# Optimization experiments

Measured on AMD Instinct MI355X. Metric: run time of the kernel, lower is better.

Reference implementation:

```python
import jax, jax.numpy as jnp
import numpy as np

N_LAYERS = 4
GAMMA = 0.5
D_MODEL = 256
D_STATE = 64
D_CONV = 4
EXPAND = 2
D_INNER = EXPAND * D_MODEL            # 512 (= headdim, so nheads = 1)
NHEADS = 1
CONV_DIM = D_INNER + 2 * D_STATE      # 640
D_IN_PROJ = 2 * D_INNER + 2 * D_STATE + NHEADS  # 1153
VOCAB = 100
VOCAB_PAD = 104                        # padded to multiple of 8 by MambaConfig
BATCH = 8
SEQ = 2048


def setup_inputs() -> dict:
    key = jax.random.key(0)
    ks = jax.random.split(key, 8)
    def nrm(k, shape):
        # gamma init: std = 1 / d1**gamma, d1 = shape[0]
        return (jax.random.normal(k, shape, jnp.float32) * (1.0 / shape[0] ** GAMMA))
    inp = {}
    inp["input_ids"] = jax.random.randint(ks[0], (BATCH, SEQ), 0, VOCAB)
    inp["embed"] = nrm(ks[1], (VOCAB_PAD, D_MODEL))          # tied embedding / lm_head
    inp["in_proj_w"] = nrm(ks[2], (N_LAYERS * D_IN_PROJ, D_MODEL)).reshape(N_LAYERS, D_IN_PROJ, D_MODEL)
    inp["conv_w"] = nrm(ks[3], (N_LAYERS * CONV_DIM, D_CONV)).reshape(N_LAYERS, CONV_DIM, D_CONV)
    inp["conv_b"] = jnp.zeros((N_LAYERS, CONV_DIM), jnp.float32)
    inp["dt_bias"] = jax.random.uniform(ks[4], (N_LAYERS, NHEADS), jnp.float32, -4.0, -1.0)
    inp["A_log"] = jnp.log(jax.random.uniform(ks[5], (N_LAYERS, NHEADS), jnp.float32, 1.0, 16.0))
    inp["Dparam"] = jnp.ones((N_LAYERS, NHEADS), jnp.float32)
    inp["norm_g_w"] = jnp.ones((N_LAYERS, D_INNER), jnp.float32)
    inp["out_proj_w"] = nrm(ks[6], (N_LAYERS * D_MODEL, D_INNER)).reshape(N_LAYERS, D_MODEL, D_INNER)
    inp["block_norm_w"] = jnp.ones((N_LAYERS, D_MODEL), jnp.float32)
    inp["norm_f_w"] = jnp.ones((D_MODEL,), jnp.float32)
    return inp


def rmsnorm(x, w, eps=1e-5):
    return x * jax.lax.rsqrt(jnp.mean(x * x, axis=-1, keepdims=True) + eps) * w


def ssm_scan(x, dt, A, Bc, Cc):
    # x: (B,L,P)  dt: (B,L)  A: scalar  Bc,Cc: (B,L,N). Sequential selective scan.
    def step(h, inp):  # h: (B,P,N)
        x_t, dt_t, b_t, c_t = inp
        h = h * jnp.exp(dt_t * A)[:, None, None] + (dt_t[:, None] * x_t)[:, :, None] * b_t[:, None, :]
        y = jnp.einsum('bpn,bn->bp', h, c_t)
        return h, y
    h0 = jnp.zeros((x.shape[0], x.shape[2], Bc.shape[2]), x.dtype)
    xs = (jnp.swapaxes(x, 0, 1), jnp.swapaxes(dt, 0, 1), jnp.swapaxes(Bc, 0, 1), jnp.swapaxes(Cc, 0, 1))
    _, ys = jax.lax.scan(step, h0, xs)
    return jnp.swapaxes(ys, 0, 1)  # (B,L,P)


def mamba2_mixer(h, ipw, cw, cb, dtb, alog, dp, ngw, opw):
    zxbcdt = h @ ipw.T                                   # (B,L,1153)
    z = zxbcdt[..., :D_INNER]
    xBC = zxbcdt[..., D_INNER:D_INNER + CONV_DIM]
    dt_raw = zxbcdt[..., D_INNER + CONV_DIM:]            # (B,L,1)
    # depthwise causal conv1d (kernel D_CONV) + SiLU
    xp = jnp.pad(xBC, ((0, 0), (D_CONV - 1, 0), (0, 0)))
    L = xBC.shape[1]
    conv = sum(xp[:, k:k + L, :] * cw[:, k] for k in range(D_CONV)) + cb
    xBC = jax.nn.silu(conv)
    x = xBC[..., :D_INNER]
    Bc = xBC[..., D_INNER:D_INNER + D_STATE]
    Cc = xBC[..., D_INNER + D_STATE:]
    dt = jax.nn.softplus(dt_raw[..., 0] + dtb[0])        # (B,L), nheads=1
    A = -jnp.exp(alog[0])
    y = ssm_scan(x, dt, A, Bc, Cc) + dp[0] * x
    y = rmsnorm(y * jax.nn.silu(z), ngw)                 # RMSNormGated (norm after gate)
    return y @ opw.T


def reference(input_ids, embed, in_proj_w, conv_w, conv_b, dt_bias, A_log, Dparam,
              norm_g_w, out_proj_w, block_norm_w, norm_f_w):
    hidden = embed[input_ids]                            # (B,L,D_MODEL)
    residual = None
    for i in range(N_LAYERS):
        residual = hidden if residual is None else hidden + residual
        hidden = rmsnorm(residual, block_norm_w[i])
        hidden = mamba2_mixer(hidden, in_proj_w[i], conv_w[i], conv_b[i], dt_bias[i],
                              A_log[i], Dparam[i], norm_g_w[i], out_proj_w[i])
    residual = hidden + residual
    final = rmsnorm(residual, norm_f_w)
    logits = final @ embed.T                             # tied lm_head, (B,L,VOCAB_PAD)
    return logits[:, -1, :VOCAB]                         # last-token logits, (B,VOCAB)
```

## Files before the change

kernel.cpp:

```cpp
#include <hip/hip_runtime.h>
#include <math.h>

#define NB    8
#define LSEQ  2048
#define TKN   16384
#define DM    256
#define DI    512
#define DS    64
#define DIP   1153
#define DIPP  1160
#define CDIM  640
#define NL    4
#define NC    16
#define CL    128
#define VOC   100

typedef short bf16x8 __attribute__((ext_vector_type(8)));
typedef short bf16x4 __attribute__((ext_vector_type(4)));
typedef float f32x4  __attribute__((ext_vector_type(4)));
typedef unsigned short ushort_t;

__device__ __forceinline__ float block_reduce_sum256(float v) {
  __shared__ float sred[4];
  #pragma unroll
  for (int off = 32; off > 0; off >>= 1) v += __shfl_down(v, off, 64);
  int lane = threadIdx.x & 63, wid = threadIdx.x >> 6;
  if (lane == 0) sred[wid] = v;
  __syncthreads();
  return sred[0] + sred[1] + sred[2] + sred[3];
}

__device__ __forceinline__ unsigned short f2bf(float f) {
  unsigned int u = __float_as_uint(f);
  unsigned int r = u + 0x7FFFu + ((u >> 16) & 1u);
  return (unsigned short)(r >> 16);
}
__device__ __forceinline__ float bf2f(unsigned short u) {
  return __uint_as_float(((unsigned int)u) << 16);
}

__global__ __launch_bounds__(256) void convert_w(const float* __restrict__ ipw,
    const float* __restrict__ opw, ushort_t* __restrict__ wbi, ushort_t* __restrict__ wbo) {
  const int n1 = NL * DIP * DM;
  const int n2 = NL * DM * DI;
  int i4 = (blockIdx.x * 256 + threadIdx.x) * 4;
  if (i4 < n1) {
    float4 v = *(const float4*)(ipw + i4);
    bf16x4 o; o[0] = (short)f2bf(v.x); o[1] = (short)f2bf(v.y);
    o[2] = (short)f2bf(v.z); o[3] = (short)f2bf(v.w);
    *(bf16x4*)(wbi + i4) = o;
  } else {
    int j = i4 - n1;
    if (j < n2) {
      float4 v = *(const float4*)(opw + j);
      bf16x4 o; o[0] = (short)f2bf(v.x); o[1] = (short)f2bf(v.y);
      o[2] = (short)f2bf(v.z); o[3] = (short)f2bf(v.w);
      *(bf16x4*)(wbo + j) = o;
    }
  }
}

__global__ __launch_bounds__(256) void embed_rmsnorm(float* __restrict__ resid,
    ushort_t* __restrict__ hn, const float* __restrict__ w,
    const int* __restrict__ ids, const float* __restrict__ embed) {
  int wave = threadIdx.x >> 6, lane = threadIdx.x & 63;
  int t = blockIdx.x * 4 + wave;
  size_t o = (size_t)t * DM + lane * 4;
  int id = ids[t];
  float4 r4 = *(const float4*)&embed[(size_t)id * DM + lane * 4];
  *(float4*)&resid[o] = r4;
  float ss = r4.x * r4.x + r4.y * r4.y + r4.z * r4.z + r4.w * r4.w;
  #pragma unroll
  for (int m = 32; m >= 1; m >>= 1) ss += __shfl_xor(ss, m, 64);
  float sc = rsqrtf(ss * (1.f / DM) + 1e-5f);
  float4 w4 = *(const float4*)&w[lane * 4];
  bf16x4 o4;
  o4[0] = (short)f2bf(r4.x * sc * w4.x);
  o4[1] = (short)f2bf(r4.y * sc * w4.y);
  o4[2] = (short)f2bf(r4.z * sc * w4.z);
  o4[3] = (short)f2bf(r4.w * sc * w4.w);
  *(bf16x4*)&hn[o] = o4;
}

#define LSTR  40
#define LSTR2 72
__global__ __launch_bounds__(256) void gemm_nt_bf16(const ushort_t* __restrict__ A,
    const ushort_t* __restrict__ Bw, ushort_t* __restrict__ C, int N, int K, int ldc) {
  __shared__ short sA[128 * LSTR2];
  __shared__ short sB[128 * LSTR2];
  int tid = threadIdx.x;
  int bn = blockIdx.x * 128;
  int bm = blockIdx.y * 128;
  int wave = tid >> 6, lane = tid & 63;
  int wm = (wave >> 1) * 64, wn = (wave & 1) * 64;
  int q = lane >> 4, c = lane & 15;

  f32x4 acc[4][4];
  #pragma unroll
  for (int i = 0; i < 4; ++i)
    #pragma unroll
    for (int j = 0; j < 4; ++j) acc[i][j] = (f32x4)0.f;

  int sr = tid >> 1;
  int sc = (tid & 1) * 32;
  const ushort_t* Ag = A + (size_t)(bm + sr) * K + sc;
  const ushort_t* Bg = Bw + (size_t)(bn + sr) * K + sc;
  bool bok = (bn + sr) < N;
  short* sAp = &sA[sr * LSTR2 + sc];
  short* sBp = &sB[sr * LSTR2 + sc];

  for (int k0 = 0; k0 < K; k0 += 64) {
    bf16x8 a0 = *(const bf16x8*)(Ag + k0);
    bf16x8 a1 = *(const bf16x8*)(Ag + k0 + 8);
    bf16x8 a2 = *(const bf16x8*)(Ag + k0 + 16);
    bf16x8 a3 = *(const bf16x8*)(Ag + k0 + 24);
    bf16x8 b0 = (bf16x8)(short)0, b1 = (bf16x8)(short)0;
    bf16x8 b2 = (bf16x8)(short)0, b3 = (bf16x8)(short)0;
    if (bok) {
      b0 = *(const bf16x8*)(Bg + k0);
      b1 = *(const bf16x8*)(Bg + k0 + 8);
      b2 = *(const bf16x8*)(Bg + k0 + 16);
      b3 = *(const bf16x8*)(Bg + k0 + 24);
    }
    __syncthreads();
    *(bf16x8*)(sAp)      = a0;
    *(bf16x8*)(sAp + 8)  = a1;
    *(bf16x8*)(sAp + 16) = a2;
    *(bf16x8*)(sAp + 24) = a3;
    *(bf16x8*)(sBp)      = b0;
    *(bf16x8*)(sBp + 8)  = b1;
    *(bf16x8*)(sBp + 16) = b2;
    *(bf16x8*)(sBp + 24) = b3;
    __syncthreads();
    #pragma unroll
    for (int ks = 0; ks < 2; ++ks) {
      bf16x8 af[4], bfr[4];
      #pragma unroll
      for (int i = 0; i < 4; ++i)
        af[i] = *(const bf16x8*)&sA[(wm + i * 16 + c) * LSTR2 + ks * 32 + q * 8];
      #pragma unroll
      for (int j = 0; j < 4; ++j)
        bfr[j] = *(const bf16x8*)&sB[(wn + j * 16 + c) * LSTR2 + ks * 32 + q * 8];
      #pragma unroll
      for (int i = 0; i < 4; ++i)
        #pragma unroll
        for (int j = 0; j < 4; ++j)
          acc[i][j] = __builtin_amdgcn_mfma_f32_16x16x32_bf16(af[i], bfr[j], acc[i][j], 0, 0, 0);
    }
  }
  #pragma unroll
  for (int i = 0; i < 4; ++i) {
    int m = bm + wm + i * 16 + q * 4;
    #pragma unroll
    for (int j = 0; j < 4; ++j) {
      int n = bn + wn + j * 16 + c;
      if (n < N) {
        #pragma unroll
        for (int r = 0; r < 4; ++r)
          C[(size_t)(m + r) * ldc + n] = f2bf(acc[i][j][r]);
      }
    }
  }
}

__global__ __launch_bounds__(256) void outproj_norm(const ushort_t* __restrict__ yb,
    const ushort_t* __restrict__ zx, const ushort_t* __restrict__ Bw,
    const float* __restrict__ gw, float* __restrict__ resid,
    const float* __restrict__ wnext, ushort_t* __restrict__ hn) {
  __shared__ short sA[32 * LSTR];
  __shared__ short sB[256 * LSTR];
  __shared__ float swl[DI];
  __shared__ float swn[DM];
  __shared__ float rs[128];
  __shared__ float rs2[32 * 2];
  int tid = threadIdx.x;
  int bm = blockIdx.x * 32;
  int wave = tid >> 6, lane = tid & 63;
  int wm = (wave >> 1) * 16, wn = (wave & 1) * 128;
  int q = lane >> 4, c = lane & 15;
  swl[tid] = gw[tid];
  swl[tid + 256] = gw[tid + 256];
  swn[tid] = wnext[tid];

  f32x4 acc[8];
  #pragma unroll
  for (int j = 0; j < 8; ++j) acc[j] = (f32x4)0.f;

  int ar = tid >> 2, ak = (tid & 3) * 8;
  bool isa = tid < 128;
  const ushort_t* yrow = yb + (size_t)(bm + ar) * DI + ak;
  const ushort_t* zrow = zx + (size_t)(bm + ar) * DIPP + ak;
  const ushort_t* Bg = Bw + (size_t)tid * DI;
  float sumsq = 0.f;
  __syncthreads();

  for (int k0 = 0; k0 < DI; k0 += 32) {
    bf16x8 g8;
    if (isa) {
      bf16x8 y8 = *(const bf16x8*)(yrow + k0);
      bf16x8 z8 = *(const bf16x8*)(zrow + k0);
      #pragma unroll
      for (int e = 0; e < 8; ++e) {
        float zz = bf2f((ushort_t)z8[e]);
        float gg = bf2f((ushort_t)y8[e]) * (zz / (1.f + __expf(-zz)));
        sumsq += gg * gg;
        g8[e] = (short)f2bf(gg * swl[k0 + ak + e]);
      }
    }
    bf16x8 b0 = *(const bf16x8*)(Bg + k0);
    bf16x8 b1 = *(const bf16x8*)(Bg + k0 + 8);
    bf16x8 b2 = *(const bf16x8*)(Bg + k0 + 16);
    bf16x8 b3 = *(const bf16x8*)(Bg + k0 + 24);
    __syncthreads();
    if (isa) *(bf16x8*)&sA[ar * LSTR + ak] = g8;
    *(bf16x8*)&sB[tid * LSTR]      = b0;
    *(bf16x8*)&sB[tid * LSTR + 8]  = b1;
    *(bf16x8*)&sB[tid * LSTR + 16] = b2;
    *(bf16x8*)&sB[tid * LSTR + 24] = b3;
    __syncthreads();
    bf16x8 af = *(const bf16x8*)&sA[(wm + c) * LSTR + q * 8];
    #pragma unroll
    for (int j = 0; j < 8; ++j) {
      bf16x8 bfr = *(const bf16x8*)&sB[(wn + j * 16 + c) * LSTR + q * 8];
      acc[j] = __builtin_amdgcn_mfma_f32_16x16x32_bf16(af, bfr, acc[j], 0, 0, 0);
    }
  }
  if (isa) rs[tid] = sumsq;
  __syncthreads();

  float outv[8][4];
  float sq2[4];
  #pragma unroll
  for (int r = 0; r < 4; ++r) {
    int row = wm + q * 4 + r;
    float s1 = rsqrtf((rs[row * 4] + rs[row * 4 + 1] + rs[row * 4 + 2] + rs[row * 4 + 3])
                      * (1.f / DI) + 1e-5f);
    float sq = 0.f;
    #pragma unroll
    for (int j = 0; j < 8; ++j) {
      int col = wn + j * 16 + c;
      size_t ro = (size_t)(bm + row) * DM + col;
      float rn = resid[ro] + s1 * acc[j][r];
      resid[ro] = rn;
      outv[j][r] = rn;
      sq += rn * rn;
    }
    sq2[r] = sq;
  }
  #pragma unroll
  for (int r = 0; r < 4; ++r) {
    #pragma unroll
    for (int m = 1; m <= 8; m <<= 1) sq2[r] += __shfl_xor(sq2[r], m, 64);
  }
  if (c == 0) {
    #pragma unroll
    for (int r = 0; r < 4; ++r)
      rs2[(wm + q * 4 + r) * 2 + (wave & 1)] = sq2[r];
  }
  __syncthreads();
  #pragma unroll
  for (int r = 0; r < 4; ++r) {
    int row = wm + q * 4 + r;
    float s2 = rsqrtf((rs2[row * 2] + rs2[row * 2 + 1]) * (1.f / DM) + 1e-5f);
    #pragma unroll
    for (int j = 0; j < 8; ++j) {
      int col = wn + j * 16 + c;
      hn[(size_t)(bm + row) * DM + col] = f2bf(outv[j][r] * s2 * swn[col]);
    }
  }
}

__global__ __launch_bounds__(256) void conv_silu(const ushort_t* __restrict__ zx,
    const float* __restrict__ cw, const float* __restrict__ cb,
    const float* __restrict__ dtb, ushort_t* __restrict__ xo,
    ushort_t* __restrict__ Bo, ushort_t* __restrict__ Co, ushort_t* __restrict__ Ut) {
  __shared__ ushort_t tile[67 * 128];
  __shared__ ushort_t tt[128 * 72];
  __shared__ float sdt[64];
  int tid = threadIdx.x;
  int ct = blockIdx.x, tb_ = blockIdx.y, b = blockIdx.z;
  int c0 = ct * 128, l0 = tb_ * 64;
  size_t rowb = (size_t)b * LSEQ;
  bool isx = (ct < 4);
  for (int slot = tid; slot < 67 * 16; slot += 256) {
    int r = slot >> 4, gg = slot & 15;
    int l = l0 + r - 3;
    bf16x8 v = (bf16x8)(short)0;
    if (l >= 0) v = *(const bf16x8*)&zx[(rowb + l) * DIPP + DI + c0 + gg * 8];
    *(bf16x8*)&tile[r * 128 + gg * 8] = v;
  }
  if (isx && tid < 64) sdt[tid] = dtb[rowb + l0 + tid];
  int g = tid & 15, tq = tid >> 4;
  int cbase = c0 + g * 8;
  float w[4][8], bias[8];
  #pragma unroll
  for (int e = 0; e < 8; ++e) {
    float4 wv = *(const float4*)&cw[(cbase + e) * 4];
    w[0][e] = wv.x; w[1][e] = wv.y; w[2][e] = wv.z; w[3][e] = wv.w;
    bias[e] = cb[cbase + e];
  }
  __syncthreads();
  bf16x8 rows[7];
  #pragma unroll
  for (int r = 0; r < 7; ++r)
    rows[r] = *(const bf16x8*)&tile[(tq * 4 + r) * 128 + g * 8];
  #pragma unroll
  for (int it = 0; it < 4; ++it) {
    int t = tq * 4 + it;
    size_t tl = rowb + l0 + t;
    float dtv = isx ? sdt[t] : 0.f;
    bf16x8 o;
    #pragma unroll
    for (int e = 0; e < 8; ++e) {
      float s = bias[e]
              + w[0][e] * bf2f((ushort_t)rows[it][e])
              + w[1][e] * bf2f((ushort_t)rows[it + 1][e])
              + w[2][e] * bf2f((ushort_t)rows[it + 2][e])
              + w[3][e] * bf2f((ushort_t)rows[it + 3][e]);
      float v = s / (1.f + __expf(-s));
      o[e] = (short)f2bf(v);
      if (isx) tt[(g * 8 + e) * 72 + t] = f2bf(v * dtv);
    }
    if (isx) {
      *(bf16x8*)&xo[tl * DI + cbase] = o;
    } else if (g < 8) {
      *(bf16x8*)&Bo[tl * DS + (cbase - DI)] = o;
    } else {
      *(bf16x8*)&Co[tl * DS + (cbase - DI - DS)] = o;
    }
  }
  if (isx) {
    __syncthreads();
    #pragma unroll
    for (int pass = 0; pass < 4; ++pass) {
      int slot = pass * 256 + tid;
      int op = slot >> 3, sg = slot & 7;
      bf16x8 v = *(const bf16x8*)&tt[op * 72 + sg * 8];
      *(bf16x8*)&Ut[((size_t)b * DI + c0 + op) * LSEQ + l0 + sg * 8] = v;
    }
  }
}

__global__ __launch_bounds__(256) void csum_k(const ushort_t* __restrict__ zx,
    const float* __restrict__ dtbias, float* __restrict__ dtb, float* __restrict__ csumb) {
  int tid = threadIdx.x;
  int wave = tid >> 6, lane = tid & 63;
  int cg = blockIdx.x * 4 + wave;
  int b = cg >> 4, ch = cg & 15;
  size_t base = (size_t)b * LSEQ + ch * CL;
  float bias = dtbias[0];
  float x0 = bf2f(zx[(base + 2 * lane) * DIPP + (DIP - 1)]) + bias;
  float x1 = bf2f(zx[(base + 2 * lane + 1) * DIPP + (DIP - 1)]) + bias;
  float d0 = (x0 > 20.f) ? x0 : log1pf(__expf(x0));
  float d1 = (x1 > 20.f) ? x1 : log1pf(__expf(x1));
  dtb[base + 2 * lane] = d0;
  dtb[base + 2 * lane + 1] = d1;
  float p = d0 + d1;
  #pragma unroll
  for (int off = 1; off < 64; off <<= 1) {
    float t = __shfl_up(p, off, 64);
    if (lane >= off) p += t;
  }
  csumb[base + 2 * lane]     = p - d1;
  csumb[base + 2 * lane + 1] = p;
}

__global__ __launch_bounds__(256) void state_gemm(const ushort_t* __restrict__ Bb,
    const ushort_t* __restrict__ Ut, const float* __restrict__ csumb,
    const float* __restrict__ alog, float* __restrict__ hst) {
  __shared__ short sW[64 * 144];
  __shared__ short sX[128 * 40];
  __shared__ float scs[128];
  int tid = threadIdx.x;
  int ph = blockIdx.x, ch = blockIdx.y, b = blockIdx.z;
  int bc = b * NC + ch;
  size_t tb = (size_t)b * LSEQ + ch * CL;
  float Aval = -expf(alog[0]);
  if (tid < 128) scs[tid] = csumb[tb + tid];
  __syncthreads();
  float Stot = scs[127];
  {
    int s = tid >> 1, noff = (tid & 1) * 32;
    float scale = __expf(Aval * (Stot - scs[s]));
    #pragma unroll
    for (int blk = 0; blk < 4; ++blk) {
      bf16x8 v = *(const bf16x8*)&Bb[(tb + s) * DS + noff + blk * 8];
      #pragma unroll
      for (int e = 0; e < 8; ++e)
        sW[(noff + blk * 8 + e) * 144 + s] = (short)f2bf(bf2f((ushort_t)v[e]) * scale);
    }
  }
  int wave = tid >> 6, lane = tid & 63;
  int wn = (wave >> 1) * 32, wp = (wave & 1) * 64;
  int q = lane >> 4, c = lane & 15;
  f32x4 acc[2][4];
  #pragma unroll
  for (int i = 0; i < 2; ++i)
    #pragma unroll
    for (int j = 0; j < 4; ++j) acc[i][j] = (f32x4)0.f;

  for (int ks = 0; ks < 4; ++ks) {
    __syncthreads();
    {
      int r = tid >> 1, off = (tid & 1) * 16;
      size_t ua = ((size_t)b * DI + ph * 128 + r) * LSEQ + ch * CL + ks * 32 + off;
      bf16x8 u0 = *(const bf16x8*)&Ut[ua];
      bf16x8 u1 = *(const bf16x8*)&Ut[ua + 8];
      *(bf16x8*)&sX[r * 40 + off]     = u0;
      *(bf16x8*)&sX[r * 40 + off + 8] = u1;
    }
    __syncthreads();
    bf16x8 af[2], bfr[4];
    #pragma unroll
    for (int i = 0; i < 2; ++i)
      af[i] = *(const bf16x8*)&sW[(wn + i * 16 + c) * 144 + ks * 32 + q * 8];
    #pragma unroll
    for (int j = 0; j < 4; ++j)
      bfr[j] = *(const bf16x8*)&sX[(wp + j * 16 + c) * 40 + q * 8];
    #pragma unroll
    for (int i = 0; i < 2; ++i)
      #pragma unroll
      for (int j = 0; j < 4; ++j)
        acc[i][j] = __builtin_amdgcn_mfma_f32_16x16x32_bf16(af[i], bfr[j], acc[i][j], 0, 0, 0);
  }
  #pragma unroll
  for (int i = 0; i < 2; ++i) {
    int n = wn + i * 16 + q * 4;
    #pragma unroll
    for (int j = 0; j < 4; ++j) {
      int pg = ph * 128 + wp + j * 16 + c;
      #pragma unroll
      for (int r = 0; r < 4; ++r)
        hst[((size_t)bc * DS + n + r) * DI + pg] = acc[i][j][r];
    }
  }
}

__global__ __launch_bounds__(256) void combine2(const float* __restrict__ hst,
    const float* __restrict__ csumb, const float* __restrict__ alog,
    ushort_t* __restrict__ hin) {
  __shared__ ushort_t ts[64 * 17];
  int tid = threadIdx.x;
  int pt = blockIdx.x, nt = blockIdx.y, b = blockIdx.z;
  int p0 = pt * 64, n0 = nt * 16;
  int pl = tid & 63, ng = tid >> 6;
  float Aval = -expf(alog[0]);
  float h[4];
  #pragma unroll
  for (int i = 0; i < 4; ++i) h[i] = 0.f;
  for (int c = 0; c < NC; ++c) {
    int bc = b * NC + c;
    #pragma unroll
    for (int i = 0; i < 4; ++i)
      ts[pl * 17 + ng * 4 + i] = f2bf(h[i]);
    __syncthreads();
    {
      int on = tid & 15;
      #pragma unroll
      for (int pass = 0; pass < 4; ++pass) {
        int op = (tid >> 4) + pass * 16;
        hin[((size_t)bc * DI + p0 + op) * DS + n0 + on] = ts[op * 17 + on];
      }
    }
    __syncthreads();
    float Sc = csumb[(size_t)b * LSEQ + c * CL + CL - 1];
    float dec = __expf(Aval * Sc);
    #pragma unroll
    for (int i = 0; i < 4; ++i) {
      float loc = hst[((size_t)bc * DS + n0 + ng * 4 + i) * DI + p0 + pl];
      h[i] = h[i] * dec + loc;
    }
  }
}

__global__ __launch_bounds__(256) void y_gemm(const ushort_t* __restrict__ Bb,
    const ushort_t* __restrict__ Cb, const ushort_t* __restrict__ Ut,
    const ushort_t* __restrict__ hin, const float* __restrict__ csumb,
    const float* __restrict__ alog, const float* __restrict__ dpar,
    const ushort_t* __restrict__ xb, ushort_t* __restrict__ y) {
  __shared__ short sC[128 * 72];
  __shared__ short sM[128 * 136];
  __shared__ short sU[128 * 80];
  __shared__ float scs[128];
  int tid = threadIdx.x;
  int ph = blockIdx.x, ch = blockIdx.y, b = blockIdx.z;
  int bc = b * NC + ch;
  size_t tb = (size_t)b * LSEQ + ch * CL;
  float Aval = -expf(alog[0]);
  float dp = dpar[0];
  int wave = tid >> 6, lane = tid & 63;
  int q = lane >> 4, c = lane & 15;

  {
    int r = tid >> 1, off = (tid & 1) * 32;
    #pragma unroll
    for (int blk = 0; blk < 4; ++blk) {
      *(bf16x8*)&sC[r * 72 + off + blk * 8] = *(const bf16x8*)&Cb[(tb + r) * DS + off + blk * 8];
      *(bf16x8*)&sU[r * 80 + off + blk * 8] = *(const bf16x8*)&Bb[(tb + r) * DS + off + blk * 8];
    }
  }
  if (tid < 128) scs[tid] = csumb[tb + tid];
  __syncthreads();

  {
    int wm = (wave >> 1) * 64, wss = (wave & 1) * 64;
    if (wave == 1) {
      #pragma unroll
      for (int i = 0; i < 4; ++i) {
        #pragma unroll
        for (int r = 0; r < 4; ++r) {
          int t = i * 16 + q * 4 + r;
          #pragma unroll
          for (int j = 0; j < 4; ++j)
            sM[t * 136 + 64 + j * 16 + c] = 0;
        }
      }
    } else {
      f32x4 g[4][4];
      #pragma unroll
      for (int i = 0; i < 4; ++i)
        #pragma unroll
        for (int j = 0; j < 4; ++j) g[i][j] = (f32x4)0.f;
      #pragma unroll
      for (int k0 = 0; k0 < 64; k0 += 32) {
        bf16x8 af[4], bfr[4];
        #pragma unroll
        for (int i = 0; i < 4; ++i)
          af[i] = *(const bf16x8*)&sC[(wm + i * 16 + c) * 72 + k0 + q * 8];
        #pragma unroll
        for (int j = 0; j < 4; ++j)
          bfr[j] = *(const bf16x8*)&sU[(wss + j * 16 + c) * 80 + k0 + q * 8];
        #pragma unroll
        for (int i = 0; i < 4; ++i)
          #pragma unroll
          for (int j = 0; j < 4; ++j)
            g[i][j] = __builtin_amdgcn_mfma_f32_16x16x32_bf16(af[i], bfr[j], g[i][j], 0, 0, 0);
      }
      #pragma unroll
      for (int i = 0; i < 4; ++i) {
        #pragma unroll
        for (int r = 0; r < 4; ++r) {
          int t = wm + i * 16 + q * 4 + r;
          float ct = scs[t];
          #pragma unroll
          for (int j = 0; j < 4; ++j) {
            int s = wss + j * 16 + c;
            float v = g[i][j][r];
            float m = (s <= t) ? v * __expf(Aval * (ct - scs[s])) : 0.f;
            sM[t * 136 + s] = (short)f2bf(m);
          }
        }
      }
    }
  }

  int wm2 = (wave >> 1) * 64, wp = (wave & 1) * 64;
  f32x4 acc[4][4];
  #pragma unroll
  for (int i = 0; i < 4; ++i)
    #pragma unroll
    for (int j = 0; j < 4; ++j) acc[i][j] = (f32x4)0.f;

  for (int ks = 0; ks < 4; ++ks) {
    __syncthreads();
    {
      int r = tid >> 1, off = (tid & 1) * 16;
      size_t ua = ((size_t)b * DI + ph * 128 + r) * LSEQ + ch * CL + ks * 32 + off;
      bf16x8 u0 = *(const bf16x8*)&Ut[ua];
      bf16x8 u1 = *(const bf16x8*)&Ut[ua + 8];
      *(bf16x8*)&sU[r * 40 + off]     = u0;
      *(bf16x8*)&sU[r * 40 + off + 8] = u1;
    }
    __syncthreads();
    if (!(wm2 == 0 && ks >= 2)) {
      bf16x8 af[4], bfr[4];
      #pragma unroll
      for (int i = 0; i < 4; ++i)
        af[i] = *(const bf16x8*)&sM[(wm2 + i * 16 + c) * 136 + ks * 32 + q * 8];
      #pragma unroll
      for (int j = 0; j < 4; ++j)
        bfr[j] = *(const bf16x8*)&sU[(wp + j * 16 + c) * 40 + q * 8];
      #pragma unroll
      for (int i = 0; i < 4; ++i)
        #pragma unroll
        for (int j = 0; j < 4; ++j)
          acc[i][j] = __builtin_amdgcn_mfma_f32_16x16x32_bf16(af[i], bfr[j], acc[i][j], 0, 0, 0);
    }
  }

  __syncthreads();
  {
    int r = tid >> 1, off = (tid & 1) * 32;
    float sc_t = __expf(Aval * scs[r]);
    #pragma unroll
    for (int blk = 0; blk < 4; ++blk) {
      bf16x8 v = *(const bf16x8*)&sC[r * 72 + off + blk * 8];
      bf16x8 o;
      #pragma unroll
      for (int e = 0; e < 8; ++e)
        o[e] = (short)f2bf(bf2f((ushort_t)v[e]) * sc_t);
      *(bf16x8*)&sM[r * 80 + off + blk * 8] = o;
    }
  }
  for (int ks = 4; ks < 6; ++ks) {
    __syncthreads();
    {
      int r = tid >> 1, off = (tid & 1) * 16;
      size_t ha = ((size_t)bc * DI + ph * 128 + r) * DS + (ks - 4) * 32 + off;
      bf16x8 h0 = *(const bf16x8*)&hin[ha];
      bf16x8 h1 = *(const bf16x8*)&hin[ha + 8];
      *(bf16x8*)&sU[r * 40 + off]     = h0;
      *(bf16x8*)&sU[r * 40 + off + 8] = h1;
    }
    __syncthreads();
    bf16x8 af[4], bfr[4];
    #pragma unroll
    for (int i = 0; i < 4; ++i)
      af[i] = *(const bf16x8*)&sM[(wm2 + i * 16 + c) * 80 + (ks - 4) * 32 + q * 8];
    #pragma unroll
    for (int j = 0; j < 4; ++j)
      bfr[j] = *(const bf16x8*)&sU[(wp + j * 16 + c) * 40 + q * 8];
    #pragma unroll
    for (int i = 0; i < 4; ++i)
      #pragma unroll
      for (int j = 0; j < 4; ++j)
        acc[i][j] = __builtin_amdgcn_mfma_f32_16x16x32_bf16(af[i], bfr[j], acc[i][j], 0, 0, 0);
  }

  #pragma unroll
  for (int i = 0; i < 4; ++i) {
    #pragma unroll
    for (int r = 0; r < 4; ++r) {
      int t = wm2 + i * 16 + q * 4 + r;
      size_t row = (tb + t) * DI;
      #pragma unroll
      for (int j = 0; j < 4; ++j) {
        int pg = ph * 128 + wp + j * 16 + c;
        y[row + pg] = f2bf(acc[i][j][r] + dp * bf2f(xb[row + pg]));
      }
    }
  }
}

__global__ __launch_bounds__(256) void finalize(const ushort_t* __restrict__ hn,
    const float* __restrict__ embed, float* __restrict__ out) {
  int b = blockIdx.x, tid = threadIdx.x;
  __shared__ float fin[DM];
  size_t off = ((size_t)b * LSEQ + (LSEQ - 1)) * DM;
  fin[tid] = bf2f(hn[off + tid]);
  __syncthreads();
  if (tid < VOC) {
    float acc = 0.f;
    #pragma unroll 8
    for (int d = 0; d < DM; ++d) acc += fin[d] * embed[(size_t)tid * DM + d];
    out[b * VOC + tid] = acc;
  }
}

extern "C" void kernel_launch(void* const* d_in, const int* in_sizes, int n_in,
                              void* d_out, int out_size, void* d_ws, size_t ws_size,
                              hipStream_t stream) {
  const int*   ids   = (const int*)d_in[0];
  const float* embed = (const float*)d_in[1];
  const float* ipw   = (const float*)d_in[2];
  const float* cw    = (const float*)d_in[3];
  const float* cb    = (const float*)d_in[4];
  const float* dtbias= (const float*)d_in[5];
  const float* alog  = (const float*)d_in[6];
  const float* dpar  = (const float*)d_in[7];
  const float* ngw   = (const float*)d_in[8];
  const float* opw   = (const float*)d_in[9];
  const float* bnw   = (const float*)d_in[10];
  const float* nfw   = (const float*)d_in[11];
  float* out = (float*)d_out;

  char* p = (char*)d_ws;
  float* resid = (float*)p;            p += (size_t)TKN * DM * 4;
  ushort_t* hn = (ushort_t*)p;         p += (size_t)TKN * DM * 2;
  ushort_t* zx = (ushort_t*)p;         p += (size_t)TKN * DIPP * 2;
  float* dtb   = (float*)p;            p += (size_t)TKN * 4;
  float* csumb = (float*)p;            p += (size_t)TKN * 4;
  ushort_t* xb = (ushort_t*)p;         p += (size_t)TKN * DI * 2;
  ushort_t* yb = (ushort_t*)p;         p += (size_t)TKN * DI * 2;
  ushort_t* Bb = (ushort_t*)p;         p += (size_t)TKN * DS * 2;
  ushort_t* Cb = (ushort_t*)p;         p += (size_t)TKN * DS * 2;
  ushort_t* Ut = (ushort_t*)p;         p += (size_t)TKN * DI * 2;
  ushort_t* hin= (ushort_t*)p;         p += (size_t)NB * NC * DI * DS * 2;
  ushort_t* wbi= (ushort_t*)p;         p += (size_t)NL * DIP * DM * 2;
  ushort_t* wbo= (ushort_t*)p;         p += (size_t)NL * DM * DI * 2;
  float* hst = (float*)yb;

  convert_w<<<(NL * DIP * DM + NL * DM * DI + 1023) / 1024, 256, 0, stream>>>(
      ipw, opw, wbi, wbo);
  embed_rmsnorm<<<TKN / 4, 256, 0, stream>>>(resid, hn, bnw, ids, embed);

  for (int i = 0; i < NL; ++i) {
    gemm_nt_bf16<<<dim3((DIP + 127) / 128, TKN / 128), 256, 0, stream>>>(
        hn, wbi + (size_t)i * DIP * DM, zx, DIP, DM, DIPP);
    csum_k<<<32, 256, 0, stream>>>(zx, dtbias + i, dtb, csumb);
    conv_silu<<<dim3(CDIM / 128, LSEQ / 64, NB), 256, 0, stream>>>(
        zx, cw + (size_t)i * CDIM * 4, cb + (size_t)i * CDIM, dtb, xb, Bb, Cb, Ut);
    state_gemm<<<dim3(4, NC, NB), 256, 0, stream>>>(Bb, Ut, csumb, alog + i, hst);
    combine2<<<dim3(DI / 64, 4, NB), 256, 0, stream>>>(hst, csumb, alog + i, hin);
    y_gemm<<<dim3(4, NC, NB), 256, 0, stream>>>(Bb, Cb, Ut, hin, csumb, alog + i,
                                                dpar + i, xb, yb);
    const float* wnext = (i < NL - 1) ? (bnw + (size_t)(i + 1) * DM) : nfw;
    outproj_norm<<<TKN / 32, 256, 0, stream>>>(
        yb, zx, wbo + (size_t)i * DM * DI, ngw + (size_t)i * DI, resid, wnext, hn);
  }

  finalize<<<NB, 256, 0, stream>>>(hn, embed, out);
}
```

Baseline: 562.5 us.

## Fold dt cumsum into conv kernel and merge prologue kernels

The weight-conversion and embedding+RMSNorm kernels become one prologue launch. The separate dt softplus/cumsum kernel becomes extra blocks inside conv_silu. To remove the ordering dependency between them, the dt scaling moves out of the transposed x buffer and into state_gemm (state scale) and y_gemm (intra-chunk mask), which now read dt per position. This saves five kernel launches and their serialisation gaps, at the cost of some idle blocks in the conv grid and a slightly different bf16 rounding point for x*dt.

```diff
diff --git a/kernel.cpp b/kernel.cpp
--- a/kernel.cpp
+++ b/kernel.cpp
@@ -20,16 +20,6 @@
 typedef float f32x4  __attribute__((ext_vector_type(4)));
 typedef unsigned short ushort_t;
 
-__device__ __forceinline__ float block_reduce_sum256(float v) {
-  __shared__ float sred[4];
-  #pragma unroll
-  for (int off = 32; off > 0; off >>= 1) v += __shfl_down(v, off, 64);
-  int lane = threadIdx.x & 63, wid = threadIdx.x >> 6;
-  if (lane == 0) sred[wid] = v;
-  __syncthreads();
-  return sred[0] + sred[1] + sred[2] + sred[3];
-}
-
 __device__ __forceinline__ unsigned short f2bf(float f) {
   unsigned int u = __float_as_uint(f);
   unsigned int r = u + 0x7FFFu + ((u >> 16) & 1u);
@@ -39,47 +29,48 @@
   return __uint_as_float(((unsigned int)u) << 16);
 }
 
-__global__ __launch_bounds__(256) void convert_w(const float* __restrict__ ipw,
-    const float* __restrict__ opw, ushort_t* __restrict__ wbi, ushort_t* __restrict__ wbo) {
-  const int n1 = NL * DIP * DM;
-  const int n2 = NL * DM * DI;
-  int i4 = (blockIdx.x * 256 + threadIdx.x) * 4;
-  if (i4 < n1) {
-    float4 v = *(const float4*)(ipw + i4);
-    bf16x4 o; o[0] = (short)f2bf(v.x); o[1] = (short)f2bf(v.y);
-    o[2] = (short)f2bf(v.z); o[3] = (short)f2bf(v.w);
-    *(bf16x4*)(wbi + i4) = o;
+__global__ __launch_bounds__(256) void prologue(const float* __restrict__ ipw,
+    const float* __restrict__ opw, ushort_t* __restrict__ wbi, ushort_t* __restrict__ wbo,
+    const int* __restrict__ ids, const float* __restrict__ embed,
+    float* __restrict__ resid, ushort_t* __restrict__ hn, const float* __restrict__ w0) {
+  int blk = blockIdx.x;
+  if (blk < TKN / 4) {
+    int wave = threadIdx.x >> 6, lane = threadIdx.x & 63;
+    int t = blk * 4 + wave;
+    size_t o = (size_t)t * DM + lane * 4;
+    int id = ids[t];
+    float4 r4 = *(const float4*)&embed[(size_t)id * DM + lane * 4];
+    *(float4*)&resid[o] = r4;
+    float ss = r4.x * r4.x + r4.y * r4.y + r4.z * r4.z + r4.w * r4.w;
+    #pragma unroll
+    for (int m = 32; m >= 1; m >>= 1) ss += __shfl_xor(ss, m, 64);
+    float sc = rsqrtf(ss * (1.f / DM) + 1e-5f);
+    float4 w4 = *(const float4*)&w0[lane * 4];
+    bf16x4 o4;
+    o4[0] = (short)f2bf(r4.x * sc * w4.x);
+    o4[1] = (short)f2bf(r4.y * sc * w4.y);
+    o4[2] = (short)f2bf(r4.z * sc * w4.z);
+    o4[3] = (short)f2bf(r4.w * sc * w4.w);
+    *(bf16x4*)&hn[o] = o4;
   } else {
-    int j = i4 - n1;
-    if (j < n2) {
-      float4 v = *(const float4*)(opw + j);
+    const int n1 = NL * DIP * DM;
+    const int n2 = NL * DM * DI;
+    int i4 = ((blk - TKN / 4) * 256 + threadIdx.x) * 4;
+    if (i4 < n1) {
+      float4 v = *(const float4*)(ipw + i4);
       bf16x4 o; o[0] = (short)f2bf(v.x); o[1] = (short)f2bf(v.y);
       o[2] = (short)f2bf(v.z); o[3] = (short)f2bf(v.w);
-      *(bf16x4*)(wbo + j) = o;
-    }
-  }
-}
-
-__global__ __launch_bounds__(256) void embed_rmsnorm(float* __restrict__ resid,
-    ushort_t* __restrict__ hn, const float* __restrict__ w,
-    const int* __restrict__ ids, const float* __restrict__ embed) {
-  int wave = threadIdx.x >> 6, lane = threadIdx.x & 63;
-  int t = blockIdx.x * 4 + wave;
-  size_t o = (size_t)t * DM + lane * 4;
-  int id = ids[t];
-  float4 r4 = *(const float4*)&embed[(size_t)id * DM + lane * 4];
-  *(float4*)&resid[o] = r4;
-  float ss = r4.x * r4.x + r4.y * r4.y + r4.z * r4.z + r4.w * r4.w;
-  #pragma unroll
-  for (int m = 32; m >= 1; m >>= 1) ss += __shfl_xor(ss, m, 64);
-  float sc = rsqrtf(ss * (1.f / DM) + 1e-5f);
-  float4 w4 = *(const float4*)&w[lane * 4];
-  bf16x4 o4;
-  o4[0] = (short)f2bf(r4.x * sc * w4.x);
-  o4[1] = (short)f2bf(r4.y * sc * w4.y);
-  o4[2] = (short)f2bf(r4.z * sc * w4.z);
-  o4[3] = (short)f2bf(r4.w * sc * w4.w);
-  *(bf16x4*)&hn[o] = o4;
+      *(bf16x4*)(wbi + i4) = o;
+    } else {
+      int j = i4 - n1;
+      if (j < n2) {
+        float4 v = *(const float4*)(opw + j);
+        bf16x4 o; o[0] = (short)f2bf(v.x); o[1] = (short)f2bf(v.y);
+        o[2] = (short)f2bf(v.z); o[3] = (short)f2bf(v.w);
+        *(bf16x4*)(wbo + j) = o;
+      }
+    }
+  }
 }
 
 #define LSTR  40
@@ -272,15 +263,37 @@
 
 __global__ __launch_bounds__(256) void conv_silu(const ushort_t* __restrict__ zx,
     const float* __restrict__ cw, const float* __restrict__ cb,
-    const float* __restrict__ dtb, ushort_t* __restrict__ xo,
-    ushort_t* __restrict__ Bo, ushort_t* __restrict__ Co, ushort_t* __restrict__ Ut) {
+    const float* __restrict__ dtbias, ushort_t* __restrict__ xo,
+    ushort_t* __restrict__ Bo, ushort_t* __restrict__ Co, ushort_t* __restrict__ Ut,
+    float* __restrict__ dtb, float* __restrict__ csumb) {
   __shared__ ushort_t tile[67 * 128];
   __shared__ ushort_t tt[128 * 72];
-  __shared__ float sdt[64];
   int tid = threadIdx.x;
   int ct = blockIdx.x, tb_ = blockIdx.y, b = blockIdx.z;
+  size_t rowb = (size_t)b * LSEQ;
+  if (ct == 5) {
+    if (tb_ < 16 && tid < 64) {
+      int lane = tid;
+      size_t base = rowb + (size_t)tb_ * CL;
+      float bias = dtbias[0];
+      float x0 = bf2f(zx[(base + 2 * lane) * DIPP + (DIP - 1)]) + bias;
+      float x1 = bf2f(zx[(base + 2 * lane + 1) * DIPP + (DIP - 1)]) + bias;
+      float d0 = (x0 > 20.f) ? x0 : log1pf(__expf(x0));
+      float d1 = (x1 > 20.f) ? x1 : log1pf(__expf(x1));
+      dtb[base + 2 * lane] = d0;
+      dtb[base + 2 * lane + 1] = d1;
+      float p = d0 + d1;
+      #pragma unroll
+      for (int off = 1; off < 64; off <<= 1) {
+        float t = __shfl_up(p, off, 64);
+        if (lane >= off) p += t;
+      }
+      csumb[base + 2 * lane]     = p - d1;
+      csumb[base + 2 * lane + 1] = p;
+    }
+    return;
+  }
   int c0 = ct * 128, l0 = tb_ * 64;
-  size_t rowb = (size_t)b * LSEQ;
   bool isx = (ct < 4);
   for (int slot = tid; slot < 67 * 16; slot += 256) {
     int r = slot >> 4, gg = slot & 15;
@@ -289,7 +302,6 @@
     if (l >= 0) v = *(const bf16x8*)&zx[(rowb + l) * DIPP + DI + c0 + gg * 8];
     *(bf16x8*)&tile[r * 128 + gg * 8] = v;
   }
-  if (isx && tid < 64) sdt[tid] = dtb[rowb + l0 + tid];
   int g = tid & 15, tq = tid >> 4;
   int cbase = c0 + g * 8;
   float w[4][8], bias[8];
@@ -308,7 +320,6 @@
   for (int it = 0; it < 4; ++it) {
     int t = tq * 4 + it;
     size_t tl = rowb + l0 + t;
-    float dtv = isx ? sdt[t] : 0.f;
     bf16x8 o;
     #pragma unroll
     for (int e = 0; e < 8; ++e) {
@@ -319,7 +330,7 @@
               + w[3][e] * bf2f((ushort_t)rows[it + 3][e]);
       float v = s / (1.f + __expf(-s));
       o[e] = (short)f2bf(v);
-      if (isx) tt[(g * 8 + e) * 72 + t] = f2bf(v * dtv);
+      if (isx) tt[(g * 8 + e) * 72 + t] = (ushort_t)o[e];
     }
     if (isx) {
       *(bf16x8*)&xo[tl * DI + cbase] = o;
@@ -341,47 +352,25 @@
   }
 }
 
-__global__ __launch_bounds__(256) void csum_k(const ushort_t* __restrict__ zx,
-    const float* __restrict__ dtbias, float* __restrict__ dtb, float* __restrict__ csumb) {
-  int tid = threadIdx.x;
-  int wave = tid >> 6, lane = tid & 63;
-  int cg = blockIdx.x * 4 + wave;
-  int b = cg >> 4, ch = cg & 15;
-  size_t base = (size_t)b * LSEQ + ch * CL;
-  float bias = dtbias[0];
-  float x0 = bf2f(zx[(base + 2 * lane) * DIPP + (DIP - 1)]) + bias;
-  float x1 = bf2f(zx[(base + 2 * lane + 1) * DIPP + (DIP - 1)]) + bias;
-  float d0 = (x0 > 20.f) ? x0 : log1pf(__expf(x0));
-  float d1 = (x1 > 20.f) ? x1 : log1pf(__expf(x1));
-  dtb[base + 2 * lane] = d0;
-  dtb[base + 2 * lane + 1] = d1;
-  float p = d0 + d1;
-  #pragma unroll
-  for (int off = 1; off < 64; off <<= 1) {
-    float t = __shfl_up(p, off, 64);
-    if (lane >= off) p += t;
-  }
-  csumb[base + 2 * lane]     = p - d1;
-  csumb[base + 2 * lane + 1] = p;
-}
-
 __global__ __launch_bounds__(256) void state_gemm(const ushort_t* __restrict__ Bb,
     const ushort_t* __restrict__ Ut, const float* __restrict__ csumb,
-    const float* __restrict__ alog, float* __restrict__ hst) {
+    const float* __restrict__ dtb, const float* __restrict__ alog,
+    float* __restrict__ hst) {
   __shared__ short sW[64 * 144];
   __shared__ short sX[128 * 40];
   __shared__ float scs[128];
+  __shared__ float sdt[128];
   int tid = threadIdx.x;
   int ph = blockIdx.x, ch = blockIdx.y, b = blockIdx.z;
   int bc = b * NC + ch;
   size_t tb = (size_t)b * LSEQ + ch * CL;
   float Aval = -expf(alog[0]);
-  if (tid < 128) scs[tid] = csumb[tb + tid];
+  if (tid < 128) { scs[tid] = csumb[tb + tid]; sdt[tid] = dtb[tb + tid]; }
   __syncthreads();
   float Stot = scs[127];
   {
     int s = tid >> 1, noff = (tid & 1) * 32;
-    float scale = __expf(Aval * (Stot - scs[s]));
+    float scale = __expf(Aval * (Stot - scs[s])) * sdt[s];
     #pragma unroll
     for (int blk = 0; blk < 4; ++blk) {
       bf16x8 v = *(const bf16x8*)&Bb[(tb + s) * DS + noff + blk * 8];
@@ -476,12 +465,14 @@
 __global__ __launch_bounds__(256) void y_gemm(const ushort_t* __restrict__ Bb,
     const ushort_t* __restrict__ Cb, const ushort_t* __restrict__ Ut,
     const ushort_t* __restrict__ hin, const float* __restrict__ csumb,
-    const float* __restrict__ alog, const float* __restrict__ dpar,
-    const ushort_t* __restrict__ xb, ushort_t* __restrict__ y) {
+    const float* __restrict__ dtb, const float* __restrict__ alog,
+    const float* __restrict__ dpar, const ushort_t* __restrict__ xb,
+    ushort_t* __restrict__ y) {
   __shared__ short sC[128 * 72];
   __shared__ short sM[128 * 136];
   __shared__ short sU[128 * 80];
   __shared__ float scs[128];
+  __shared__ float sdt[128];
   int tid = threadIdx.x;
   int ph = blockIdx.x, ch = blockIdx.y, b = blockIdx.z;
   int bc = b * NC + ch;
@@ -499,7 +490,7 @@
       *(bf16x8*)&sU[r * 80 + off + blk * 8] = *(const bf16x8*)&Bb[(tb + r) * DS + off + blk * 8];
     }
   }
-  if (tid < 128) scs[tid] = csumb[tb + tid];
+  if (tid < 128) { scs[tid] = csumb[tb + tid]; sdt[tid] = dtb[tb + tid]; }
   __syncthreads();
 
   {
@@ -536,6 +527,9 @@
           for (int j = 0; j < 4; ++j)
             g[i][j] = __builtin_amdgcn_mfma_f32_16x16x32_bf16(af[i], bfr[j], g[i][j], 0, 0, 0);
       }
+      float dts[4];
+      #pragma unroll
+      for (int j = 0; j < 4; ++j) dts[j] = sdt[wss + j * 16 + c];
       #pragma unroll
       for (int i = 0; i < 4; ++i) {
         #pragma unroll
@@ -546,7 +540,7 @@
           for (int j = 0; j < 4; ++j) {
             int s = wss + j * 16 + c;
             float v = g[i][j][r];
-            float m = (s <= t) ? v * __expf(Aval * (ct - scs[s])) : 0.f;
+            float m = (s <= t) ? v * __expf(Aval * (ct - scs[s])) * dts[j] : 0.f;
             sM[t * 136 + s] = (short)f2bf(m);
           }
         }
@@ -690,20 +684,20 @@
   ushort_t* wbo= (ushort_t*)p;         p += (size_t)NL * DM * DI * 2;
   float* hst = (float*)yb;
 
-  convert_w<<<(NL * DIP * DM + NL * DM * DI + 1023) / 1024, 256, 0, stream>>>(
-      ipw, opw, wbi, wbo);
-  embed_rmsnorm<<<TKN / 4, 256, 0, stream>>>(resid, hn, bnw, ids, embed);
+  const int convblks = (NL * DIP * DM + NL * DM * DI + 1023) / 1024;
+  prologue<<<TKN / 4 + convblks, 256, 0, stream>>>(ipw, opw, wbi, wbo,
+                                                   ids, embed, resid, hn, bnw);
 
   for (int i = 0; i < NL; ++i) {
     gemm_nt_bf16<<<dim3((DIP + 127) / 128, TKN / 128), 256, 0, stream>>>(
         hn, wbi + (size_t)i * DIP * DM, zx, DIP, DM, DIPP);
-    csum_k<<<32, 256, 0, stream>>>(zx, dtbias + i, dtb, csumb);
-    conv_silu<<<dim3(CDIM / 128, LSEQ / 64, NB), 256, 0, stream>>>(
-        zx, cw + (size_t)i * CDIM * 4, cb + (size_t)i * CDIM, dtb, xb, Bb, Cb, Ut);
-    state_gemm<<<dim3(4, NC, NB), 256, 0, stream>>>(Bb, Ut, csumb, alog + i, hst);
+    conv_silu<<<dim3(6, LSEQ / 64, NB), 256, 0, stream>>>(
+        zx, cw + (size_t)i * CDIM * 4, cb + (size_t)i * CDIM, dtbias + i,
+        xb, Bb, Cb, Ut, dtb, csumb);
+    state_gemm<<<dim3(4, NC, NB), 256, 0, stream>>>(Bb, Ut, csumb, dtb, alog + i, hst);
     combine2<<<dim3(DI / 64, 4, NB), 256, 0, stream>>>(hst, csumb, alog + i, hin);
-    y_gemm<<<dim3(4, NC, NB), 256, 0, stream>>>(Bb, Cb, Ut, hin, csumb, alog + i,
-                                                dpar + i, xb, yb);
+    y_gemm<<<dim3(4, NC, NB), 256, 0, stream>>>(Bb, Cb, Ut, hin, csumb, dtb,
+                                                alog + i, dpar + i, xb, yb);
     const float* wnext = (i < NL - 1) ? (bnw + (size_t)(i + 1) * DM) : nfw;
     outproj_norm<<<TKN / 32, 256, 0, stream>>>(
         yb, zx, wbo + (size_t)i * DM * DI, ngw + (size_t)i * DI, resid, wnext, hn);
```

Result: faster. 544.0 us (median of 2 runs) (-3.3%).
